# Performance work log

Hardware: AMD Instinct MI355X
Metric: run time of the kernel (lower is better)

Reference implementation:

```python
import jax, jax.numpy as jnp
import numpy as np

B, S, D, V = 2, 2048, 4096, 32000

def setup_inputs() -> dict:
    key = jax.random.key(0)
    k1, k2, k3 = jax.random.split(key, 3)
    hidden_states = jax.random.normal(k1, (B, S, D), dtype=jnp.float32)
    W = jax.random.normal(k2, (V, D), dtype=jnp.float32) * 0.02  # lm_head weight [vocab, hidden]
    label_ids = jax.random.randint(k3, (B, S), 0, V, dtype=jnp.int64)
    return {"hidden_states": hidden_states, "W": W, "label_ids": label_ids}

def reference(hidden_states, W, label_ids):
    # lm_head: Linear(D, V, bias=False) -> logits [B, S, V], cast to fp32
    logits = jnp.einsum('bsd,vd->bsv', hidden_states, W).astype(jnp.float32)
    # shift: predict token t+1 from position t
    shift_logits = logits[:, :-1, :].reshape(-1, V)          # [B*(S-1), V]
    shift_labels = label_ids[:, 1:].reshape(-1)              # [B*(S-1)]
    logp = jax.nn.log_softmax(shift_logits, axis=-1)
    nll = -jnp.take_along_axis(logp, shift_labels[:, None], axis=1)[:, 0]
    loss = jnp.mean(nll)  # CrossEntropyLoss default reduction='mean'
    return loss, logits
```

## Files before the change

### kernel.cpp

```cpp
#include <hip/hip_runtime.h>
#include <hip/hip_bf16.h>

#define M_ 4096
#define N_ 32000
#define K_ 4096
#define S_ 2048
#define SM1 2047
#define NROWS 4094
#define NT_ 64

typedef __bf16 bf16x8 __attribute__((ext_vector_type(8)));
typedef float f32x4 __attribute__((ext_vector_type(4)));

#define GLDS16(g, l)                                                         \
  __builtin_amdgcn_global_load_lds(                                          \
      (__attribute__((address_space(1))) const void*)(g),                    \
      (__attribute__((address_space(3))) void*)(l), 16, 0, 0)
#define BAR() __builtin_amdgcn_s_barrier()
#define PRIO1() __builtin_amdgcn_s_setprio(1)
#define PRIO0() __builtin_amdgcn_s_setprio(0)
#define VMCNT(n) asm volatile("s_waitcnt vmcnt(" #n ")" ::: "memory")
#define LGKM0() asm volatile("s_waitcnt lgkmcnt(0)" ::: "memory")

__global__ __launch_bounds__(256) void cvt_f32_to_bf16(
    const float* __restrict__ in, bf16x8* __restrict__ out, long n8) {
  long i0 = (long)blockIdx.x * blockDim.x + threadIdx.x;
  long stride = (long)gridDim.x * blockDim.x;
  for (long i = i0; i < n8; i += stride) {
    const float4* p = reinterpret_cast<const float4*>(in) + i * 2;
    float4 a = p[0];
    float4 b = p[1];
    bf16x8 v;
    v[0] = (__bf16)a.x; v[1] = (__bf16)a.y; v[2] = (__bf16)a.z; v[3] = (__bf16)a.w;
    v[4] = (__bf16)b.x; v[5] = (__bf16)b.y; v[6] = (__bf16)b.z; v[7] = (__bf16)b.w;
    out[i] = v;
  }
}

__global__ __launch_bounds__(512, 2) void gemm256(
    const __bf16* __restrict__ A, const __bf16* __restrict__ B,
    float* __restrict__ C) {
  __shared__ __align__(1024) unsigned char smem[2][65536];

  const int tid = threadIdx.x;
  const int bid = blockIdx.x;
  const int wg = (bid & 7) * 250 + (bid >> 3);
  const int nblk = wg >> 4;
  const int mblk = wg & 15;
  const int m0 = mblk * 256;
  const int n0 = nblk * 256;

  const int w = tid >> 6;
  const int lane = tid & 63;
  const int wm = w >> 2;
  const int wn = w & 3;
  const int rl = lane & 15;
  const int cl = lane >> 4;
  const int srow = tid >> 3;
  const int sc = (tid & 7) ^ (srow & 7);
  const int sdst = tid * 16;

  f32x4 acc[8][4];
#pragma unroll
  for (int i = 0; i < 8; ++i)
#pragma unroll
    for (int j = 0; j < 4; ++j) acc[i][j] = (f32x4){0.f, 0.f, 0.f, 0.f};

  auto stA = [&](int nbuf, int kt, int r0) {
    GLDS16(A + (size_t)(m0 + r0 + srow) * K_ + kt * 64 + sc * 8,
           &smem[nbuf][r0 * 128 + sdst]);
  };
  auto stB = [&](int nbuf, int kt, int r0) {
    GLDS16(B + (size_t)(n0 + r0 + srow) * K_ + kt * 64 + sc * 8,
           &smem[nbuf][32768 + r0 * 128 + sdst]);
  };
  auto ld = [&](const unsigned char* base, int row, int c) -> bf16x8 {
    return *(const bf16x8*)(base + row * 128 + ((c ^ (row & 7)) << 4));
  };

  stA(0, 0, 0); stA(0, 0, 128);
  stB(0, 0, 0); stB(0, 0, 64); stB(0, 0, 128); stB(0, 0, 192);
  stA(0, 0, 64); stA(0, 0, 192);
  VMCNT(2);
  BAR();

  bf16x8 a[4][2], b0[2][2], b1[2][2];
  for (int s = 0; s < NT_; ++s) {
    const int cur = s & 1;
    const int nxt = cur ^ 1;
    const unsigned char* bA = smem[cur];
    const unsigned char* bB = smem[cur] + 32768;
    const bool st = (s + 1 < NT_);
    const int k1 = s + 1;

#pragma unroll
    for (int ii = 0; ii < 4; ++ii)
#pragma unroll
      for (int ks = 0; ks < 2; ++ks)
        a[ii][ks] = ld(bA, wm * 128 + ii * 16 + rl, ks * 4 + cl);
#pragma unroll
    for (int jj = 0; jj < 2; ++jj)
#pragma unroll
      for (int ks = 0; ks < 2; ++ks)
        b0[jj][ks] = ld(bB, wn * 64 + jj * 16 + rl, ks * 4 + cl);
    if (st) { stA(nxt, k1, 0); stA(nxt, k1, 128); }
    BAR();
    LGKM0();
    PRIO1();
#pragma unroll
    for (int ii = 0; ii < 4; ++ii)
#pragma unroll
      for (int jj = 0; jj < 2; ++jj)
#pragma unroll
        for (int ks = 0; ks < 2; ++ks)
          acc[ii][jj] = __builtin_amdgcn_mfma_f32_16x16x32_bf16(
              a[ii][ks], b0[jj][ks], acc[ii][jj], 0, 0, 0);
    PRIO0();
    BAR();

#pragma unroll
    for (int jj = 0; jj < 2; ++jj)
#pragma unroll
      for (int ks = 0; ks < 2; ++ks)
        b1[jj][ks] = ld(bB, wn * 64 + 32 + jj * 16 + rl, ks * 4 + cl);
    if (st) { stB(nxt, k1, 0); stB(nxt, k1, 64); }
    BAR();
    LGKM0();
    PRIO1();
#pragma unroll
    for (int ii = 0; ii < 4; ++ii)
#pragma unroll
      for (int jj = 0; jj < 2; ++jj)
#pragma unroll
        for (int ks = 0; ks < 2; ++ks)
          acc[ii][2 + jj] = __builtin_amdgcn_mfma_f32_16x16x32_bf16(
              a[ii][ks], b1[jj][ks], acc[ii][2 + jj], 0, 0, 0);
    PRIO0();
    if (st) { VMCNT(4); } else { VMCNT(0); }
    BAR();

#pragma unroll
    for (int ii = 0; ii < 4; ++ii)
#pragma unroll
      for (int ks = 0; ks < 2; ++ks)
        a[ii][ks] = ld(bA, wm * 128 + 64 + ii * 16 + rl, ks * 4 + cl);
    if (st) { stB(nxt, k1, 128); stB(nxt, k1, 192); }
    BAR();
    LGKM0();
    PRIO1();
#pragma unroll
    for (int ii = 0; ii < 4; ++ii)
#pragma unroll
      for (int jj = 0; jj < 2; ++jj)
#pragma unroll
        for (int ks = 0; ks < 2; ++ks)
          acc[4 + ii][jj] = __builtin_amdgcn_mfma_f32_16x16x32_bf16(
              a[ii][ks], b0[jj][ks], acc[4 + ii][jj], 0, 0, 0);
    PRIO0();
    BAR();

    if (st) { stA(nxt, k1, 64); stA(nxt, k1, 192); }
    BAR();
    PRIO1();
#pragma unroll
    for (int ii = 0; ii < 4; ++ii)
#pragma unroll
      for (int jj = 0; jj < 2; ++jj)
#pragma unroll
        for (int ks = 0; ks < 2; ++ks)
          acc[4 + ii][2 + jj] = __builtin_amdgcn_mfma_f32_16x16x32_bf16(
              a[ii][ks], b1[jj][ks], acc[4 + ii][2 + jj], 0, 0, 0);
    PRIO0();
    if (st) { VMCNT(2); }
    BAR();
  }

#pragma unroll
  for (int i = 0; i < 8; ++i)
#pragma unroll
    for (int j = 0; j < 4; ++j)
#pragma unroll
      for (int r = 0; r < 4; ++r) {
        const int grow = m0 + wm * 128 + i * 16 + cl * 4 + r;
        const int gcol = n0 + wn * 64 + j * 16 + rl;
        C[(size_t)grow * N_ + gcol] = acc[i][j][r];
      }
}

__global__ __launch_bounds__(256) void gemm_fb(const float* __restrict__ Ap,
                                               const float* __restrict__ Bp,
                                               float* __restrict__ Cp) {
  __shared__ __align__(1024) unsigned char smem[2][16384];
  const int tid = threadIdx.x;
  const int bid = blockIdx.x;
  const int swz = (bid & 7) * 1000 + (bid >> 3);
  const int nblk = swz >> 5;
  const int mblk = swz & 31;
  const int m0 = mblk * 128;
  const int n0 = nblk * 128;
  const int w = tid >> 6, lane = tid & 63;
  const int wm = w >> 1, wn = w & 1;
  const int rl = lane & 15, cl = lane >> 4;

  f32x4 acc[4][4];
#pragma unroll
  for (int i = 0; i < 4; ++i)
#pragma unroll
    for (int j = 0; j < 4; ++j) acc[i][j] = (f32x4){0.f, 0.f, 0.f, 0.f};

  auto stage = [&](int buf, int kt) {
    const int k0 = kt * 32;
#pragma unroll
    for (int j = 0; j < 2; ++j) {
      const int t = j * 256 + tid;
      const int row = t >> 2;
      const int c = t & 3;
      const int rp = row >> 1;
      const int pp = ((row & 1) * 4 + c) ^ (rp & 7);
      const int lb = rp * 128 + pp * 16;
      {
        const float4* g = (const float4*)(Ap + (size_t)(m0 + row) * K_ + k0 + c * 8);
        float4 x = g[0], y = g[1];
        bf16x8 v;
        v[0] = (__bf16)x.x; v[1] = (__bf16)x.y; v[2] = (__bf16)x.z; v[3] = (__bf16)x.w;
        v[4] = (__bf16)y.x; v[5] = (__bf16)y.y; v[6] = (__bf16)y.z; v[7] = (__bf16)y.w;
        *(bf16x8*)(&smem[buf][lb]) = v;
      }
      {
        const float4* g = (const float4*)(Bp + (size_t)(n0 + row) * K_ + k0 + c * 8);
        float4 x = g[0], y = g[1];
        bf16x8 v;
        v[0] = (__bf16)x.x; v[1] = (__bf16)x.y; v[2] = (__bf16)x.z; v[3] = (__bf16)x.w;
        v[4] = (__bf16)y.x; v[5] = (__bf16)y.y; v[6] = (__bf16)y.z; v[7] = (__bf16)y.w;
        *(bf16x8*)(&smem[buf][8192 + lb]) = v;
      }
    }
  };
  auto ldfrag = [&](const unsigned char* base, int row, int c) -> bf16x8 {
    const int rp = row >> 1;
    const int pp = ((row & 1) * 4 + c) ^ (rp & 7);
    return *(const bf16x8*)(base + rp * 128 + pp * 16);
  };
  auto compute = [&](int buf) {
    const unsigned char* bA = smem[buf];
    const unsigned char* bB = smem[buf] + 8192;
    bf16x8 af[4], bfv[4];
#pragma unroll
    for (int i = 0; i < 4; ++i) af[i] = ldfrag(bA, wm * 64 + i * 16 + rl, cl);
#pragma unroll
    for (int j = 0; j < 4; ++j) bfv[j] = ldfrag(bB, wn * 64 + j * 16 + rl, cl);
#pragma unroll
    for (int i = 0; i < 4; ++i)
#pragma unroll
      for (int j = 0; j < 4; ++j)
        acc[i][j] = __builtin_amdgcn_mfma_f32_16x16x32_bf16(af[i], bfv[j],
                                                            acc[i][j], 0, 0, 0);
  };

  stage(0, 0);
  __syncthreads();
  for (int kt = 0; kt < 128; kt += 2) {
    if (kt + 1 < 128) stage(1, kt + 1);
    compute(0);
    __syncthreads();
    if (kt + 2 < 128) stage(0, kt + 2);
    compute(1);
    __syncthreads();
  }
#pragma unroll
  for (int i = 0; i < 4; ++i)
#pragma unroll
    for (int j = 0; j < 4; ++j)
#pragma unroll
      for (int r = 0; r < 4; ++r) {
        const int grow = m0 + wm * 64 + i * 16 + cl * 4 + r;
        const int gcol = n0 + wn * 64 + j * 16 + rl;
        Cp[(size_t)grow * N_ + gcol] = acc[i][j][r];
      }
}

__device__ __forceinline__ float wred_max(float v) {
#pragma unroll
  for (int o = 32; o > 0; o >>= 1) v = fmaxf(v, __shfl_xor(v, o));
  return v;
}
__device__ __forceinline__ float wred_sum(float v) {
#pragma unroll
  for (int o = 32; o > 0; o >>= 1) v += __shfl_xor(v, o);
  return v;
}

__global__ __launch_bounds__(256) void ce_rows(const float* __restrict__ logits,
                                               const int* __restrict__ labels,
                                               float* __restrict__ nll) {
  const int r = blockIdx.x;
  const int b = r / SM1;
  const int t = r - b * SM1;
  const float* row = logits + (size_t)(b * S_ + t) * N_;
  const int lane = threadIdx.x & 63;
  const int w = threadIdx.x >> 6;
  __shared__ float red[8];

  float m = -3.4e38f;
  for (int v = threadIdx.x; v < N_; v += 256) m = fmaxf(m, row[v]);
  float wm_ = wred_max(m);
  if (lane == 0) red[w] = wm_;
  __syncthreads();
  m = fmaxf(fmaxf(red[0], red[1]), fmaxf(red[2], red[3]));

  float s = 0.f;
  for (int v = threadIdx.x; v < N_; v += 256) s += __expf(row[v] - m);
  float ws = wred_sum(s);
  if (lane == 0) red[4 + w] = ws;
  __syncthreads();
  if (threadIdx.x == 0) {
    const float tot = red[4] + red[5] + red[6] + red[7];
    const int lbl = labels[b * S_ + t + 1];
    nll[r] = m + __logf(tot) - row[lbl];
  }
}

__global__ __launch_bounds__(256) void reduce_loss(const float* __restrict__ nll,
                                                   float* __restrict__ out) {
  float s = 0.f;
  for (int i = threadIdx.x; i < NROWS; i += 256) s += nll[i];
  s = wred_sum(s);
  __shared__ float sb[4];
  if ((threadIdx.x & 63) == 0) sb[threadIdx.x >> 6] = s;
  __syncthreads();
  if (threadIdx.x == 0) out[0] = (sb[0] + sb[1] + sb[2] + sb[3]) / (float)NROWS;
}

extern "C" void kernel_launch(void* const* d_in, const int* in_sizes, int n_in,
                              void* d_out, int out_size, void* d_ws,
                              size_t ws_size, hipStream_t stream) {
  const float* h = (const float*)d_in[0];
  const float* Wf = (const float*)d_in[1];
  const int* labels = (const int*)d_in[2];
  float* out = (float*)d_out;
  float* logits = out + 1;

  const size_t abytes = (size_t)M_ * K_ * 2;
  const size_t bbytes = (size_t)N_ * K_ * 2;
  const size_t need = abytes + bbytes + (size_t)NROWS * sizeof(float);

  if (ws_size >= need) {
    unsigned char* base = (unsigned char*)d_ws;
    __bf16* hA = (__bf16*)base;
    __bf16* wB = (__bf16*)(base + abytes);
    float* nll = (float*)(base + abytes + bbytes);
    cvt_f32_to_bf16<<<2048, 256, 0, stream>>>(h, (bf16x8*)hA,
                                              (long)((size_t)M_ * K_ / 8));
    cvt_f32_to_bf16<<<4096, 256, 0, stream>>>(Wf, (bf16x8*)wB,
                                              (long)((size_t)N_ * K_ / 8));
    gemm256<<<2000, 512, 0, stream>>>(hA, wB, logits);
    ce_rows<<<4094, 256, 0, stream>>>(logits, labels, nll);
    reduce_loss<<<1, 256, 0, stream>>>(nll, out);
  } else {
    float* nll = (float*)d_ws;
    gemm_fb<<<8000, 256, 0, stream>>>(h, Wf, logits);
    ce_rows<<<4094, 256, 0, stream>>>(logits, labels, nll);
    reduce_loss<<<1, 256, 0, stream>>>(nll, out);
  }
}
```

Before: 1.382 ms.

## Switch GEMM to 4-stage BK=32 pipeline and single-pass online softmax CE

The bf16 GEMM now uses K tiles of 32 instead of 64 and four LDS buffers, prefetching three stages ahead in place of double buffering. Each iteration has two MFMA phases instead of four, which cuts barriers per tile but doubles the iteration count. Separately, the cross-entropy row kernel replaces its two passes over the logits with a single vectorized float4 pass using an online max/sum-exp merge, halving global reads of the large logits matrix. The online merge adds extra exp calls when the running max changes.

```diff
diff --git a/kernel.cpp b/kernel.cpp
--- a/kernel.cpp
+++ b/kernel.cpp
@@ -7,7 +7,7 @@
 #define S_ 2048
 #define SM1 2047
 #define NROWS 4094
-#define NT_ 64
+#define NT_ 128
 
 typedef __bf16 bf16x8 __attribute__((ext_vector_type(8)));
 typedef float f32x4 __attribute__((ext_vector_type(4)));
@@ -40,7 +40,7 @@
 __global__ __launch_bounds__(512, 2) void gemm256(
     const __bf16* __restrict__ A, const __bf16* __restrict__ B,
     float* __restrict__ C) {
-  __shared__ __align__(1024) unsigned char smem[2][65536];
+  __shared__ __align__(1024) unsigned char smem[4][32768];
 
   const int tid = threadIdx.x;
   const int bid = blockIdx.x;
@@ -56,9 +56,6 @@
   const int wn = w & 3;
   const int rl = lane & 15;
   const int cl = lane >> 4;
-  const int srow = tid >> 3;
-  const int sc = (tid & 7) ^ (srow & 7);
-  const int sdst = tid * 16;
 
   f32x4 acc[8][4];
 #pragma unroll
@@ -66,112 +63,74 @@
 #pragma unroll
     for (int j = 0; j < 4; ++j) acc[i][j] = (f32x4){0.f, 0.f, 0.f, 0.f};
 
-  auto stA = [&](int nbuf, int kt, int r0) {
-    GLDS16(A + (size_t)(m0 + r0 + srow) * K_ + kt * 64 + sc * 8,
-           &smem[nbuf][r0 * 128 + sdst]);
-  };
-  auto stB = [&](int nbuf, int kt, int r0) {
-    GLDS16(B + (size_t)(n0 + r0 + srow) * K_ + kt * 64 + sc * 8,
-           &smem[nbuf][32768 + r0 * 128 + sdst]);
-  };
-  auto ld = [&](const unsigned char* base, int row, int c) -> bf16x8 {
-    return *(const bf16x8*)(base + row * 128 + ((c ^ (row & 7)) << 4));
-  };
-
-  stA(0, 0, 0); stA(0, 0, 128);
-  stB(0, 0, 0); stB(0, 0, 64); stB(0, 0, 128); stB(0, 0, 192);
-  stA(0, 0, 64); stA(0, 0, 192);
-  VMCNT(2);
+  auto stA = [&](unsigned char* buf, int kt) {
+#pragma unroll
+    for (int j = 0; j < 2; ++j) {
+      const int cd = j * 512 + tid;
+      const int row = cd >> 2;
+      const int c = (cd & 3) ^ (row & 3);
+      GLDS16(A + (size_t)(m0 + row) * K_ + kt * 32 + c * 8, buf + cd * 16);
+    }
+  };
+  auto stB = [&](unsigned char* buf, int kt) {
+#pragma unroll
+    for (int j = 0; j < 2; ++j) {
+      const int cd = j * 512 + tid;
+      const int row = cd >> 2;
+      const int c = (cd & 3) ^ (row & 3);
+      GLDS16(B + (size_t)(n0 + row) * K_ + kt * 32 + c * 8,
+             buf + 16384 + cd * 16);
+    }
+  };
+  auto ld = [&](const unsigned char* base, int row) -> bf16x8 {
+    return *(const bf16x8*)(base + row * 64 + (((cl ^ row) & 3) << 4));
+  };
+
+  stA(smem[0], 0); stB(smem[0], 0);
+  stA(smem[1], 1); stB(smem[1], 1);
+  stA(smem[2], 2); stB(smem[2], 2);
+  VMCNT(8);
   BAR();
 
-  bf16x8 a[4][2], b0[2][2], b1[2][2];
+  bf16x8 a[4], b[4];
   for (int s = 0; s < NT_; ++s) {
-    const int cur = s & 1;
-    const int nxt = cur ^ 1;
-    const unsigned char* bA = smem[cur];
-    const unsigned char* bB = smem[cur] + 32768;
-    const bool st = (s + 1 < NT_);
-    const int k1 = s + 1;
-
-#pragma unroll
-    for (int ii = 0; ii < 4; ++ii)
-#pragma unroll
-      for (int ks = 0; ks < 2; ++ks)
-        a[ii][ks] = ld(bA, wm * 128 + ii * 16 + rl, ks * 4 + cl);
-#pragma unroll
-    for (int jj = 0; jj < 2; ++jj)
-#pragma unroll
-      for (int ks = 0; ks < 2; ++ks)
-        b0[jj][ks] = ld(bB, wn * 64 + jj * 16 + rl, ks * 4 + cl);
-    if (st) { stA(nxt, k1, 0); stA(nxt, k1, 128); }
+    const unsigned char* bufc = smem[s & 3];
+    unsigned char* bufn = smem[(s + 3) & 3];
+    const bool st = (s < NT_ - 3);
+
+#pragma unroll
+    for (int i = 0; i < 4; ++i) a[i] = ld(bufc, wm * 128 + i * 16 + rl);
+#pragma unroll
+    for (int j = 0; j < 4; ++j) b[j] = ld(bufc + 16384, wn * 64 + j * 16 + rl);
+    if (st) stA(bufn, s + 3);
     BAR();
     LGKM0();
     PRIO1();
 #pragma unroll
     for (int ii = 0; ii < 4; ++ii)
 #pragma unroll
-      for (int jj = 0; jj < 2; ++jj)
-#pragma unroll
-        for (int ks = 0; ks < 2; ++ks)
-          acc[ii][jj] = __builtin_amdgcn_mfma_f32_16x16x32_bf16(
-              a[ii][ks], b0[jj][ks], acc[ii][jj], 0, 0, 0);
+      for (int jj = 0; jj < 4; ++jj)
+        acc[ii][jj] = __builtin_amdgcn_mfma_f32_16x16x32_bf16(
+            a[ii], b[jj], acc[ii][jj], 0, 0, 0);
     PRIO0();
     BAR();
 
 #pragma unroll
-    for (int jj = 0; jj < 2; ++jj)
-#pragma unroll
-      for (int ks = 0; ks < 2; ++ks)
-        b1[jj][ks] = ld(bB, wn * 64 + 32 + jj * 16 + rl, ks * 4 + cl);
-    if (st) { stB(nxt, k1, 0); stB(nxt, k1, 64); }
+    for (int i = 0; i < 4; ++i) a[i] = ld(bufc, wm * 128 + 64 + i * 16 + rl);
+    if (st) stB(bufn, s + 3);
     BAR();
     LGKM0();
     PRIO1();
 #pragma unroll
     for (int ii = 0; ii < 4; ++ii)
 #pragma unroll
-      for (int jj = 0; jj < 2; ++jj)
-#pragma unroll
-        for (int ks = 0; ks < 2; ++ks)
-          acc[ii][2 + jj] = __builtin_amdgcn_mfma_f32_16x16x32_bf16(
-              a[ii][ks], b1[jj][ks], acc[ii][2 + jj], 0, 0, 0);
+      for (int jj = 0; jj < 4; ++jj)
+        acc[4 + ii][jj] = __builtin_amdgcn_mfma_f32_16x16x32_bf16(
+            a[ii], b[jj], acc[4 + ii][jj], 0, 0, 0);
     PRIO0();
-    if (st) { VMCNT(4); } else { VMCNT(0); }
-    BAR();
-
-#pragma unroll
-    for (int ii = 0; ii < 4; ++ii)
-#pragma unroll
-      for (int ks = 0; ks < 2; ++ks)
-        a[ii][ks] = ld(bA, wm * 128 + 64 + ii * 16 + rl, ks * 4 + cl);
-    if (st) { stB(nxt, k1, 128); stB(nxt, k1, 192); }
-    BAR();
-    LGKM0();
-    PRIO1();
-#pragma unroll
-    for (int ii = 0; ii < 4; ++ii)
-#pragma unroll
-      for (int jj = 0; jj < 2; ++jj)
-#pragma unroll
-        for (int ks = 0; ks < 2; ++ks)
-          acc[4 + ii][jj] = __builtin_amdgcn_mfma_f32_16x16x32_bf16(
-              a[ii][ks], b0[jj][ks], acc[4 + ii][jj], 0, 0, 0);
-    PRIO0();
-    BAR();
-
-    if (st) { stA(nxt, k1, 64); stA(nxt, k1, 192); }
-    BAR();
-    PRIO1();
-#pragma unroll
-    for (int ii = 0; ii < 4; ++ii)
-#pragma unroll
-      for (int jj = 0; jj < 2; ++jj)
-#pragma unroll
-        for (int ks = 0; ks < 2; ++ks)
-          acc[4 + ii][2 + jj] = __builtin_amdgcn_mfma_f32_16x16x32_bf16(
-              a[ii][ks], b1[jj][ks], acc[4 + ii][2 + jj], 0, 0, 0);
-    PRIO0();
-    if (st) { VMCNT(2); }
+    if (s < NT_ - 3) { VMCNT(8); }
+    else if (s == NT_ - 3) { VMCNT(4); }
+    else if (s == NT_ - 2) { VMCNT(0); }
     BAR();
   }
 
@@ -279,17 +238,6 @@
       }
 }
 
-__device__ __forceinline__ float wred_max(float v) {
-#pragma unroll
-  for (int o = 32; o > 0; o >>= 1) v = fmaxf(v, __shfl_xor(v, o));
-  return v;
-}
-__device__ __forceinline__ float wred_sum(float v) {
-#pragma unroll
-  for (int o = 32; o > 0; o >>= 1) v += __shfl_xor(v, o);
-  return v;
-}
-
 __global__ __launch_bounds__(256) void ce_rows(const float* __restrict__ logits,
                                                const int* __restrict__ labels,
                                                float* __restrict__ nll) {
@@ -297,26 +245,34 @@
   const int b = r / SM1;
   const int t = r - b * SM1;
   const float* row = logits + (size_t)(b * S_ + t) * N_;
-  const int lane = threadIdx.x & 63;
-  const int w = threadIdx.x >> 6;
-  __shared__ float red[8];
-
-  float m = -3.4e38f;
-  for (int v = threadIdx.x; v < N_; v += 256) m = fmaxf(m, row[v]);
-  float wm_ = wred_max(m);
-  if (lane == 0) red[w] = wm_;
-  __syncthreads();
-  m = fmaxf(fmaxf(red[0], red[1]), fmaxf(red[2], red[3]));
-
-  float s = 0.f;
-  for (int v = threadIdx.x; v < N_; v += 256) s += __expf(row[v] - m);
-  float ws = wred_sum(s);
-  if (lane == 0) red[4 + w] = ws;
+  float m = -3.4e38f, s = 0.f;
+  const float4* row4 = (const float4*)row;
+  for (int i = threadIdx.x; i < 7936; i += 256) {
+    float4 v = row4[i];
+    float mx = fmaxf(fmaxf(v.x, v.y), fmaxf(v.z, v.w));
+    if (mx > m) { s *= __expf(m - mx); m = mx; }
+    s += __expf(v.x - m) + __expf(v.y - m) + __expf(v.z - m) + __expf(v.w - m);
+  }
+  {
+    float v = row[31744 + threadIdx.x];
+    if (v > m) { s *= __expf(m - v); m = v; }
+    s += __expf(v - m);
+  }
+#pragma unroll
+  for (int o = 32; o > 0; o >>= 1) {
+    float m2 = __shfl_xor(m, o), s2 = __shfl_xor(s, o);
+    float mn = fmaxf(m, m2);
+    s = s * __expf(m - mn) + s2 * __expf(m2 - mn);
+    m = mn;
+  }
+  __shared__ float rm[4], rs[4];
+  if ((threadIdx.x & 63) == 0) { rm[threadIdx.x >> 6] = m; rs[threadIdx.x >> 6] = s; }
   __syncthreads();
   if (threadIdx.x == 0) {
-    const float tot = red[4] + red[5] + red[6] + red[7];
-    const int lbl = labels[b * S_ + t + 1];
-    nll[r] = m + __logf(tot) - row[lbl];
+    float M = fmaxf(fmaxf(rm[0], rm[1]), fmaxf(rm[2], rm[3]));
+    float S = rs[0] * __expf(rm[0] - M) + rs[1] * __expf(rm[1] - M) +
+              rs[2] * __expf(rm[2] - M) + rs[3] * __expf(rm[3] - M);
+    nll[r] = M + __logf(S) - row[labels[b * S_ + t + 1]];
   }
 }
 
@@ -324,7 +280,8 @@
                                                    float* __restrict__ out) {
   float s = 0.f;
   for (int i = threadIdx.x; i < NROWS; i += 256) s += nll[i];
-  s = wred_sum(s);
+#pragma unroll
+  for (int o = 32; o > 0; o >>= 1) s += __shfl_xor(s, o);
   __shared__ float sb[4];
   if ((threadIdx.x & 63) == 0) sb[threadIdx.x >> 6] = s;
   __syncthreads();
```

Measured after the change: 1.351 ms. 1.02x faster.
